# Kernel optimization log

Measured on AMD Instinct MI355X. Metric: run time of the kernel, lower is better.

The kernel has to match this reference:

```python
import jax, jax.numpy as jnp
import numpy as np

D_MODEL = 1024
EXPANDED = 1024  # d_model * expansion_factor(1.0)
K = 3
EPS = 1e-8


def rms_norm(x, w, eps=EPS):
    return x * jax.lax.rsqrt(jnp.mean(x * x, axis=-1, keepdims=True) + eps) * w


def setup_inputs() -> dict:
    key = jax.random.key(0)
    ks = jax.random.split(key, 8)
    b, t = 4, 4096
    u = jax.random.normal(ks[0], (b, t, D_MODEL), dtype=jnp.float32)
    s_in = 1.0 / np.sqrt(D_MODEL)
    s_out = 1.0 / np.sqrt(EXPANDED)
    W_in = jax.random.uniform(ks[1], (2 * EXPANDED, D_MODEL), jnp.float32, -s_in, s_in)
    b_in = jax.random.uniform(ks[2], (2 * EXPANDED,), jnp.float32, -s_in, s_in)
    in_norm_w = jnp.ones((2 * EXPANDED,), jnp.float32)
    s_conv = 1.0 / np.sqrt(K)  # groups=expanded_dim -> fan_in = K
    conv_w = jax.random.uniform(ks[3], (EXPANDED, 1, K), jnp.float32, -s_conv, s_conv)
    conv_b = jax.random.uniform(ks[4], (EXPANDED,), jnp.float32, -s_conv, s_conv)
    W_out = jax.random.uniform(ks[5], (D_MODEL, EXPANDED), jnp.float32, -s_out, s_out)
    b_out = jax.random.uniform(ks[6], (D_MODEL,), jnp.float32, -s_out, s_out)
    out_norm_w = jnp.ones((D_MODEL,), jnp.float32)
    return {
        "u": u, "W_in": W_in, "b_in": b_in, "in_norm_w": in_norm_w,
        "conv_w": conv_w, "conv_b": conv_b,
        "W_out": W_out, "b_out": b_out, "out_norm_w": out_norm_w,
    }


def reference(u, W_in, b_in, in_norm_w, conv_w, conv_b, W_out, b_out, out_norm_w):
    # in_proj + RMSNorm
    xv = rms_norm(jnp.einsum('btd,ed->bte', u, W_in) + b_in, in_norm_w)  # [b,t,2E]
    x, v = jnp.split(xv, 2, axis=-1)  # each [b,t,E]
    # depthwise 'same' conv along time: NCH layout
    x_f = jnp.transpose(x, (0, 2, 1))  # [b,E,t]
    pad = (K - 1) // 2
    y = jax.lax.conv_general_dilated(
        x_f, conv_w, window_strides=(1,), padding=[(pad, pad)],
        dimension_numbers=('NCH', 'OIH', 'NCH'), feature_group_count=EXPANDED)
    y = y + conv_b[None, :, None]
    x_mixed = jnp.transpose(y, (0, 2, 1))  # [b,t,E]
    gated = v * x_mixed
    out = rms_norm(jnp.einsum('bte,de->btd', gated, W_out) + b_out, out_norm_w)
    return out
```

## Files before the change

### kernel.cpp

```cpp
#include <hip/hip_runtime.h>

#define BT    16384
#define TSEQ  4096
#define DM    1024
#define EXP   1024
#define N1    2048
#define KDIM  1024
#define NKT   32
#define EPSV  1e-8f

typedef __bf16 bf16x8 __attribute__((ext_vector_type(8)));
typedef float f32x16 __attribute__((ext_vector_type(16)));
typedef unsigned short u16x8 __attribute__((ext_vector_type(8)));

#define AS1CAST(p) ((__attribute__((address_space(1))) void*)(p))
#define AS3CAST(p) ((__attribute__((address_space(3))) void*)(p))

__device__ __forceinline__ unsigned short f2bf(float f) {
    unsigned int u = __float_as_uint(f);
    u += 0x7fffu + ((u >> 16) & 1u);
    return (unsigned short)(u >> 16);
}

__global__ __launch_bounds__(256) void k_f2bf3(const float* __restrict__ i0, unsigned short* __restrict__ o0, int n0,
                                               const float* __restrict__ i1, unsigned short* __restrict__ o1, int n1,
                                               const float* __restrict__ i2, unsigned short* __restrict__ o2, int n2,
                                               float* __restrict__ ssq) {
    int i = blockIdx.x * 256 + threadIdx.x;
    const float* in; unsigned short* out;
    if (i < n0)                { in = i0; out = o0; }
    else if (i < n0 + n1)      { in = i1; out = o1; i -= n0; }
    else if (i < n0 + n1 + n2) { in = i2; out = o2; i -= n0 + n1; }
    else {
        i -= n0 + n1 + n2;
        if (i < 2 * BT / 4) ((float4*)ssq)[i] = make_float4(0.f, 0.f, 0.f, 0.f);
        return;
    }
    float4 v = ((const float4*)in)[i];
    ushort4 o;
    o.x = f2bf(v.x); o.y = f2bf(v.y); o.z = f2bf(v.z); o.w = f2bf(v.w);
    ((ushort4*)out)[i] = o;
}

template <int BF16_OUT, int NT>
__device__ __forceinline__ void gemm_body(const unsigned short* __restrict__ A,
                                          const unsigned short* __restrict__ Bw,
                                          const float* __restrict__ bias,
                                          unsigned short* __restrict__ Cb,
                                          float* __restrict__ Cf,
                                          float* __restrict__ ssq,
                                          int N) {
    __shared__ __align__(16) char smem[73728];

    const int tid  = threadIdx.x;
    const int lane = tid & 63;
    const int w    = tid >> 6;
    const int ln   = lane & 31;
    const int hi   = lane >> 5;

    const int L   = blockIdx.x;
    const int mt  = ((L >> 3) / NT) * 8 + (L & 7);
    const int nt  = (L >> 3) & (NT - 1);
    const int row0 = mt * 256, col0 = nt * 128;

    const int rA = tid >> 2;
    const int qS = ((tid & 3) - (tid >> 4)) & 3;
    const unsigned short* aSrc = A  + (size_t)(row0 + rA) * KDIM + qS * 8;
    const unsigned short* bSrc = Bw + (size_t)(col0 + rA) * KDIM + qS * 8;

    f32x16 acc[2][4] = {};

    auto stage = [&](int kt, unsigned short* sA, unsigned short* sB) {
#pragma unroll
        for (int b = 0; b < 4; ++b)
            __builtin_amdgcn_global_load_lds(AS1CAST(aSrc + (size_t)b * 64 * KDIM + kt * 32),
                                             AS3CAST(&sA[(b * 256 + w * 64) * 8]), 16, 0, 0);
#pragma unroll
        for (int b = 0; b < 2; ++b)
            __builtin_amdgcn_global_load_lds(AS1CAST(bSrc + (size_t)b * 64 * KDIM + kt * 32),
                                             AS3CAST(&sB[(b * 256 + w * 64) * 8]), 16, 0, 0);
    };
    auto compute = [&](const unsigned short* sA, const unsigned short* sB) {
#pragma unroll
        for (int ks = 0; ks < 2; ++ks) {
            const int sw = ((ks * 2 + hi + (ln >> 2)) & 3) * 8;
            bf16x8 aF[2], bF[4];
#pragma unroll
            for (int i = 0; i < 2; ++i)
                aF[i] = *(const bf16x8*)&sA[(w * 64 + i * 32 + ln) * 32 + sw];
#pragma unroll
            for (int j = 0; j < 4; ++j)
                bF[j] = *(const bf16x8*)&sB[(j * 32 + ln) * 32 + sw];
            __builtin_amdgcn_s_setprio(1);
#pragma unroll
            for (int i = 0; i < 2; ++i)
#pragma unroll
                for (int j = 0; j < 4; ++j)
                    acc[i][j] = __builtin_amdgcn_mfma_f32_32x32x16_bf16(
                        aF[i], bF[j], acc[i][j], 0, 0, 0);
            __builtin_amdgcn_s_setprio(0);
        }
    };

    unsigned short* A0 = (unsigned short*)smem;
    unsigned short* B0 = (unsigned short*)(smem + 16384);
    unsigned short* A1 = (unsigned short*)(smem + 24576);
    unsigned short* B1 = (unsigned short*)(smem + 40960);
    unsigned short* A2 = (unsigned short*)(smem + 49152);
    unsigned short* B2 = (unsigned short*)(smem + 65536);

    stage(0, A0, B0);
    stage(1, A1, B1);
    for (int kt = 0; kt < NKT - 1; ++kt) {
        asm volatile("s_waitcnt vmcnt(6)" ::: "memory");
        __builtin_amdgcn_s_barrier();
        if (kt + 2 < NKT) stage(kt + 2, A2, B2);
        compute(A0, B0);
        unsigned short* tA = A0; A0 = A1; A1 = A2; A2 = tA;
        unsigned short* tB = B0; B0 = B1; B1 = B2; B2 = tB;
    }
    asm volatile("s_waitcnt vmcnt(0)" ::: "memory");
    __builtin_amdgcn_s_barrier();
    compute(A0, B0);

    const int c0 = col0 + ln;
    float bs[4];
#pragma unroll
    for (int j = 0; j < 4; ++j) bs[j] = bias[c0 + j * 32];

    __syncthreads();
    float* scr = (float*)smem;

#pragma unroll
    for (int i = 0; i < 2; ++i) {
        const int lr0 = w * 64 + i * 32 + 4 * hi;
#pragma unroll
        for (int reg = 0; reg < 16; ++reg) {
            const int lr = lr0 + (reg & 3) + 8 * (reg >> 2);
            const int gm = row0 + lr;
            float v[4]; float p = 0.f;
#pragma unroll
            for (int j = 0; j < 4; ++j) {
                v[j] = acc[i][j][reg] + bs[j];
                p += v[j] * v[j];
            }
            scr[lr * 33 + ln] = p;
            size_t base = (size_t)gm * N + c0;
#pragma unroll
            for (int j = 0; j < 4; ++j) {
                if (BF16_OUT) Cb[base + j * 32] = f2bf(v[j]);
                else          Cf[base + j * 32] = v[j];
            }
        }
    }
    __syncthreads();
    float s = 0.f;
#pragma unroll
    for (int c = 0; c < 32; ++c) s += scr[tid * 33 + c];
    atomicAdd(&ssq[row0 + tid], s);
}

__global__ __launch_bounds__(256, 2) void k_gemm_in(const unsigned short* __restrict__ A,
                                                    const unsigned short* __restrict__ Bw,
                                                    const float* __restrict__ bias,
                                                    unsigned short* __restrict__ Cb,
                                                    float* __restrict__ ssq) {
    gemm_body<1, 16>(A, Bw, bias, Cb, nullptr, ssq, N1);
}

__global__ __launch_bounds__(256, 2) void k_gemm_out(const unsigned short* __restrict__ A,
                                                     const unsigned short* __restrict__ Bw,
                                                     const float* __restrict__ bias,
                                                     float* __restrict__ Cf,
                                                     float* __restrict__ ssq) {
    gemm_body<0, 8>(A, Bw, bias, nullptr, Cf, ssq, DM);
}

__global__ __launch_bounds__(256) void k_conv_gate(const unsigned short* __restrict__ z,
                                                   const float* __restrict__ ssq1,
                                                   const float* __restrict__ inw,
                                                   const float* __restrict__ cw,
                                                   const float* __restrict__ cb,
                                                   unsigned short* __restrict__ g) {
    const int tok = blockIdx.x * 2 + (threadIdx.x >> 7);
    const int e8  = (threadIdx.x & 127) * 8;
    const int t   = tok & (TSEQ - 1);

    const float rs0 = rsqrtf(ssq1[tok] * (1.0f / N1) + EPSV);
    const int tm = (t > 0) ? tok - 1 : tok;
    const int tp = (t < TSEQ - 1) ? tok + 1 : tok;
    const float rsm = (t > 0) ? rsqrtf(ssq1[tm] * (1.0f / N1) + EPSV) : 0.0f;
    const float rsp = (t < TSEQ - 1) ? rsqrtf(ssq1[tp] * (1.0f / N1) + EPSV) : 0.0f;

    bf16x8 xm = *(const bf16x8*)(z + (size_t)tm * N1 + e8);
    bf16x8 x0 = *(const bf16x8*)(z + (size_t)tok * N1 + e8);
    bf16x8 xp = *(const bf16x8*)(z + (size_t)tp * N1 + e8);
    bf16x8 vv = *(const bf16x8*)(z + (size_t)tok * N1 + EXP + e8);

    u16x8 ov;
#pragma unroll
    for (int p = 0; p < 8; ++p) {
        const int e = e8 + p;
        const float we  = inw[e];
        const float wvv = inw[EXP + e];
        const float w0 = cw[e * 3], w1 = cw[e * 3 + 1], w2 = cw[e * 3 + 2];
        float y = w0 * ((float)xm[p] * rsm * we)
                + w1 * ((float)x0[p] * rs0 * we)
                + w2 * ((float)xp[p] * rsp * we)
                + cb[e];
        float vn = (float)vv[p] * rs0 * wvv;
        ov[p] = f2bf(vn * y);
    }
    *(u16x8*)(g + (size_t)tok * EXP + e8) = ov;
}

__global__ __launch_bounds__(256) void k_outnorm(float* __restrict__ o,
                                                 const float* __restrict__ ssq2,
                                                 const float* __restrict__ onw) {
    const int idx = blockIdx.x * 256 + threadIdx.x;
    const int tok = idx >> 8;
    const int d4  = (idx & 255) * 4;
    const float rs = rsqrtf(ssq2[tok] * (1.0f / DM) + EPSV);
    float4 v = ((float4*)o)[idx];
    float4 w = *(const float4*)(onw + d4);
    v.x *= rs * w.x; v.y *= rs * w.y; v.z *= rs * w.z; v.w *= rs * w.w;
    ((float4*)o)[idx] = v;
}

extern "C" void kernel_launch(void* const* d_in, const int* in_sizes, int n_in,
                              void* d_out, int out_size, void* d_ws, size_t ws_size,
                              hipStream_t stream) {
    const float* u     = (const float*)d_in[0];
    const float* W_in  = (const float*)d_in[1];
    const float* b_in  = (const float*)d_in[2];
    const float* inw   = (const float*)d_in[3];
    const float* cw    = (const float*)d_in[4];
    const float* cb    = (const float*)d_in[5];
    const float* W_out = (const float*)d_in[6];
    const float* b_out = (const float*)d_in[7];
    const float* onw   = (const float*)d_in[8];
    float* out = (float*)d_out;

    char* ws = (char*)d_ws;
    unsigned short* u_bf    = (unsigned short*)ws; ws += (size_t)BT * DM * 2;
    unsigned short* Win_bf  = (unsigned short*)ws; ws += (size_t)N1 * DM * 2;
    unsigned short* Wout_bf = (unsigned short*)ws; ws += (size_t)DM * EXP * 2;
    unsigned short* z_bf    = (unsigned short*)ws; ws += (size_t)BT * N1 * 2;
    unsigned short* g_bf    = (unsigned short*)ws; ws += (size_t)BT * EXP * 2;
    float* ssq1 = (float*)ws; ws += (size_t)BT * 4;
    float* ssq2 = (float*)ws; ws += (size_t)BT * 4;

    const int n0 = BT * DM / 4, n1c = N1 * DM / 4, n2c = DM * EXP / 4;
    const int ntot = n0 + n1c + n2c + 2 * BT / 4;
    k_f2bf3<<<(ntot + 255) / 256, 256, 0, stream>>>(u, u_bf, n0,
                                                    W_in, Win_bf, n1c,
                                                    W_out, Wout_bf, n2c,
                                                    ssq1);

    k_gemm_in<<<(BT / 256) * (N1 / 128), 256, 0, stream>>>(u_bf, Win_bf, b_in, z_bf, ssq1);

    k_conv_gate<<<BT / 2, 256, 0, stream>>>(z_bf, ssq1, inw, cw, cb, g_bf);

    k_gemm_out<<<(BT / 256) * (DM / 128), 256, 0, stream>>>(g_bf, Wout_bf, b_out, out, ssq2);

    k_outnorm<<<BT, 256, 0, stream>>>(out, ssq2, onw);

    (void)in_sizes; (void)n_in; (void)out_size; (void)ws_size;
}
```

Before: 299.6 us.

## Fuse fp32-to-bf16 conversion of activations into input GEMM A-tile loading

```diff
diff --git a/kernel.cpp b/kernel.cpp
--- a/kernel.cpp
+++ b/kernel.cpp
@@ -6,7 +6,7 @@
 #define EXP   1024
 #define N1    2048
 #define KDIM  1024
-#define NKT   32
+#define NKT2  (KDIM / 32)
 #define EPSV  1e-8f
 
 typedef __bf16 bf16x8 __attribute__((ext_vector_type(8)));
@@ -42,15 +42,12 @@
     ((ushort4*)out)[i] = o;
 }
 
-template <int BF16_OUT, int NT>
-__device__ __forceinline__ void gemm_body(const unsigned short* __restrict__ A,
-                                          const unsigned short* __restrict__ Bw,
-                                          const float* __restrict__ bias,
-                                          unsigned short* __restrict__ Cb,
-                                          float* __restrict__ Cf,
-                                          float* __restrict__ ssq,
-                                          int N) {
-    __shared__ __align__(16) char smem[73728];
+__global__ __launch_bounds__(256, 2) void k_gemm_in(const float* __restrict__ Af,
+                                                    const unsigned short* __restrict__ Bw,
+                                                    const float* __restrict__ bias,
+                                                    unsigned short* __restrict__ Cb,
+                                                    float* __restrict__ ssq) {
+    __shared__ __align__(16) char smem[57344];
 
     const int tid  = threadIdx.x;
     const int lane = tid & 63;
@@ -59,8 +56,145 @@
     const int hi   = lane >> 5;
 
     const int L   = blockIdx.x;
-    const int mt  = ((L >> 3) / NT) * 8 + (L & 7);
-    const int nt  = (L >> 3) & (NT - 1);
+    const int mt  = ((L >> 3) / 16) * 8 + (L & 7);
+    const int nt  = (L >> 3) & 15;
+    const int row0 = mt * 256, col0 = nt * 128;
+
+    const int rA = tid >> 2;
+    const int qS = ((tid & 3) - (tid >> 4)) & 3;
+    const float*          aSrcF = Af + (size_t)(row0 + rA) * DM + qS * 8;
+    const unsigned short* bSrc  = Bw + (size_t)(col0 + rA) * KDIM + qS * 8;
+
+    auto bufAp = [&](int i) { return (unsigned short*)(smem + i * 16384); };
+    auto bufBp = [&](int i) { return (unsigned short*)(smem + 32768 + i * 8192); };
+
+    f32x16 acc[2][4] = {};
+    float4 ar[8];
+
+#define LOADA(kt_) do {                                                        \
+    _Pragma("unroll")                                                          \
+    for (int b = 0; b < 4; ++b) {                                              \
+        const float* p = aSrcF + (size_t)b * 64 * DM + (kt_) * 32;             \
+        ar[2*b]   = *(const float4*)p;                                         \
+        ar[2*b+1] = *(const float4*)(p + 4);                                   \
+    } } while (0)
+
+#define CVTWRITE(sA_) do {                                                     \
+    unsigned short* sAp_ = (sA_);                                              \
+    _Pragma("unroll")                                                          \
+    for (int b = 0; b < 4; ++b) {                                              \
+        bf16x8 t_;                                                             \
+        float4 lo_ = ar[2*b], hi_ = ar[2*b+1];                                 \
+        t_[0] = (__bf16)lo_.x; t_[1] = (__bf16)lo_.y;                          \
+        t_[2] = (__bf16)lo_.z; t_[3] = (__bf16)lo_.w;                          \
+        t_[4] = (__bf16)hi_.x; t_[5] = (__bf16)hi_.y;                          \
+        t_[6] = (__bf16)hi_.z; t_[7] = (__bf16)hi_.w;                          \
+        *(bf16x8*)&sAp_[(b * 256 + tid) * 8] = t_;                             \
+    } } while (0)
+
+    auto stageB = [&](int kt, unsigned short* sB) {
+#pragma unroll
+        for (int b = 0; b < 2; ++b)
+            __builtin_amdgcn_global_load_lds(AS1CAST(bSrc + (size_t)b * 64 * KDIM + kt * 32),
+                                             AS3CAST(&sB[(b * 256 + w * 64) * 8]), 16, 0, 0);
+    };
+    auto compute = [&](const unsigned short* sA, const unsigned short* sB) {
+#pragma unroll
+        for (int ks = 0; ks < 2; ++ks) {
+            const int sw = ((ks * 2 + hi + (ln >> 2)) & 3) * 8;
+            bf16x8 aF[2], bF[4];
+#pragma unroll
+            for (int i = 0; i < 2; ++i)
+                aF[i] = *(const bf16x8*)&sA[(w * 64 + i * 32 + ln) * 32 + sw];
+#pragma unroll
+            for (int j = 0; j < 4; ++j)
+                bF[j] = *(const bf16x8*)&sB[(j * 32 + ln) * 32 + sw];
+            __builtin_amdgcn_s_setprio(1);
+#pragma unroll
+            for (int i = 0; i < 2; ++i)
+#pragma unroll
+                for (int j = 0; j < 4; ++j)
+                    acc[i][j] = __builtin_amdgcn_mfma_f32_32x32x16_bf16(
+                        aF[i], bF[j], acc[i][j], 0, 0, 0);
+            __builtin_amdgcn_s_setprio(0);
+        }
+    };
+
+    LOADA(0);
+    stageB(0, bufBp(0));
+    stageB(1, bufBp(1));
+    CVTWRITE(bufAp(0));
+    LOADA(1);
+    asm volatile("s_waitcnt vmcnt(10)" ::: "memory");
+    asm volatile("s_waitcnt lgkmcnt(0)" ::: "memory");
+    __builtin_amdgcn_s_barrier();
+
+#pragma unroll 1
+    for (int kt = 0; kt < NKT2; ++kt) {
+        if (kt + 2 < NKT2) stageB(kt + 2, bufBp((kt + 2) % 3));
+        compute(bufAp(kt & 1), bufBp(kt % 3));
+        if (kt + 1 < NKT2) {
+            CVTWRITE(bufAp((kt + 1) & 1));
+            if (kt + 2 < NKT2) LOADA(kt + 2);
+        }
+        if (kt < NKT2 - 2) asm volatile("s_waitcnt vmcnt(8)" ::: "memory");
+        else               asm volatile("s_waitcnt vmcnt(0)" ::: "memory");
+        asm volatile("s_waitcnt lgkmcnt(0)" ::: "memory");
+        __builtin_amdgcn_s_barrier();
+    }
+#undef LOADA
+#undef CVTWRITE
+
+    const int c0 = col0 + ln;
+    float bs[4];
+#pragma unroll
+    for (int j = 0; j < 4; ++j) bs[j] = bias[c0 + j * 32];
+
+    __syncthreads();
+    float* scr = (float*)smem;
+
+#pragma unroll
+    for (int i = 0; i < 2; ++i) {
+        const int lr0 = w * 64 + i * 32 + 4 * hi;
+#pragma unroll
+        for (int reg = 0; reg < 16; ++reg) {
+            const int lr = lr0 + (reg & 3) + 8 * (reg >> 2);
+            const int gm = row0 + lr;
+            float v[4]; float p = 0.f;
+#pragma unroll
+            for (int j = 0; j < 4; ++j) {
+                v[j] = acc[i][j][reg] + bs[j];
+                p += v[j] * v[j];
+            }
+            scr[lr * 33 + ln] = p;
+            size_t base = (size_t)gm * N1 + c0;
+#pragma unroll
+            for (int j = 0; j < 4; ++j) Cb[base + j * 32] = f2bf(v[j]);
+        }
+    }
+    __syncthreads();
+    float s = 0.f;
+#pragma unroll
+    for (int c = 0; c < 32; ++c) s += scr[tid * 33 + c];
+    atomicAdd(&ssq[row0 + tid], s);
+}
+
+__global__ __launch_bounds__(256, 2) void k_gemm_out(const unsigned short* __restrict__ A,
+                                                     const unsigned short* __restrict__ Bw,
+                                                     const float* __restrict__ bias,
+                                                     float* __restrict__ Cf,
+                                                     float* __restrict__ ssq) {
+    __shared__ __align__(16) char smem[73728];
+
+    const int tid  = threadIdx.x;
+    const int lane = tid & 63;
+    const int w    = tid >> 6;
+    const int ln   = lane & 31;
+    const int hi   = lane >> 5;
+
+    const int L   = blockIdx.x;
+    const int mt  = ((L >> 3) / 8) * 8 + (L & 7);
+    const int nt  = (L >> 3) & 7;
     const int row0 = mt * 256, col0 = nt * 128;
 
     const int rA = tid >> 2;
@@ -111,10 +245,10 @@
 
     stage(0, A0, B0);
     stage(1, A1, B1);
-    for (int kt = 0; kt < NKT - 1; ++kt) {
+    for (int kt = 0; kt < NKT2 - 1; ++kt) {
         asm volatile("s_waitcnt vmcnt(6)" ::: "memory");
         __builtin_amdgcn_s_barrier();
-        if (kt + 2 < NKT) stage(kt + 2, A2, B2);
+        if (kt + 2 < NKT2) stage(kt + 2, A2, B2);
         compute(A0, B0);
         unsigned short* tA = A0; A0 = A1; A1 = A2; A2 = tA;
         unsigned short* tB = B0; B0 = B1; B1 = B2; B2 = tB;
@@ -145,12 +279,9 @@
                 p += v[j] * v[j];
             }
             scr[lr * 33 + ln] = p;
-            size_t base = (size_t)gm * N + c0;
-#pragma unroll
-            for (int j = 0; j < 4; ++j) {
-                if (BF16_OUT) Cb[base + j * 32] = f2bf(v[j]);
-                else          Cf[base + j * 32] = v[j];
-            }
+            size_t base = (size_t)gm * DM + c0;
+#pragma unroll
+            for (int j = 0; j < 4; ++j) Cf[base + j * 32] = v[j];
         }
     }
     __syncthreads();
@@ -158,22 +289,6 @@
 #pragma unroll
     for (int c = 0; c < 32; ++c) s += scr[tid * 33 + c];
     atomicAdd(&ssq[row0 + tid], s);
-}
-
-__global__ __launch_bounds__(256, 2) void k_gemm_in(const unsigned short* __restrict__ A,
-                                                    const unsigned short* __restrict__ Bw,
-                                                    const float* __restrict__ bias,
-                                                    unsigned short* __restrict__ Cb,
-                                                    float* __restrict__ ssq) {
-    gemm_body<1, 16>(A, Bw, bias, Cb, nullptr, ssq, N1);
-}
-
-__global__ __launch_bounds__(256, 2) void k_gemm_out(const unsigned short* __restrict__ A,
-                                                     const unsigned short* __restrict__ Bw,
-                                                     const float* __restrict__ bias,
-                                                     float* __restrict__ Cf,
-                                                     float* __restrict__ ssq) {
-    gemm_body<0, 8>(A, Bw, bias, nullptr, Cf, ssq, DM);
 }
 
 __global__ __launch_bounds__(256) void k_conv_gate(const unsigned short* __restrict__ z,
@@ -242,7 +357,6 @@
     float* out = (float*)d_out;
 
     char* ws = (char*)d_ws;
-    unsigned short* u_bf    = (unsigned short*)ws; ws += (size_t)BT * DM * 2;
     unsigned short* Win_bf  = (unsigned short*)ws; ws += (size_t)N1 * DM * 2;
     unsigned short* Wout_bf = (unsigned short*)ws; ws += (size_t)DM * EXP * 2;
     unsigned short* z_bf    = (unsigned short*)ws; ws += (size_t)BT * N1 * 2;
@@ -250,14 +364,14 @@
     float* ssq1 = (float*)ws; ws += (size_t)BT * 4;
     float* ssq2 = (float*)ws; ws += (size_t)BT * 4;
 
-    const int n0 = BT * DM / 4, n1c = N1 * DM / 4, n2c = DM * EXP / 4;
-    const int ntot = n0 + n1c + n2c + 2 * BT / 4;
-    k_f2bf3<<<(ntot + 255) / 256, 256, 0, stream>>>(u, u_bf, n0,
-                                                    W_in, Win_bf, n1c,
+    const int n1c = N1 * DM / 4, n2c = DM * EXP / 4;
+    const int ntot = n1c + n2c + 2 * BT / 4;
+    k_f2bf3<<<(ntot + 255) / 256, 256, 0, stream>>>(W_in, Win_bf, n1c,
                                                     W_out, Wout_bf, n2c,
+                                                    nullptr, nullptr, 0,
                                                     ssq1);
 
-    k_gemm_in<<<(BT / 256) * (N1 / 128), 256, 0, stream>>>(u_bf, Win_bf, b_in, z_bf, ssq1);
+    k_gemm_in<<<(BT / 256) * (N1 / 128), 256, 0, stream>>>(u, Win_bf, b_in, z_bf, ssq1);
 
     k_conv_gate<<<BT / 2, 256, 0, stream>>>(z_bf, ssq1, inw, cw, cb, g_bf);
 
```

After: 310.4 us. 1.04x slower.
